# Performance work log

Hardware: AMD Instinct MI355X
Metric: run time of the kernel (lower is better)

The kernel has to match this reference:

```python
import jax, jax.numpy as jnp
import numpy as np

B, N, FEAT = 4, 100000, 11
NUM_SP = 512  # superpoints per sample
H1, H2, H3, E = 128, 256, 512, 384


def setup_inputs() -> dict:
    key = jax.random.key(0)
    ks = jax.random.split(key, 10)
    s = 0.02
    return {
        "full_features": jax.random.normal(ks[0], (B, N, FEAT), dtype=jnp.float32),
        "full_super_indices": jax.random.randint(ks[1], (B, N), 0, NUM_SP, dtype=jnp.int32),
        "W1": jax.random.normal(ks[2], (H1, FEAT), dtype=jnp.float32) * s,
        "b1": jnp.zeros((H1,), jnp.float32),
        "W2": jax.random.normal(ks[3], (H2, H1), dtype=jnp.float32) * s,
        "b2": jnp.zeros((H2,), jnp.float32),
        "W3": jax.random.normal(ks[4], (H3, H3), dtype=jnp.float32) * s,
        "b3": jnp.zeros((H3,), jnp.float32),
        "W4": jax.random.normal(ks[5], (E, H3), dtype=jnp.float32) * s,
        "b4": jnp.zeros((E,), jnp.float32),
    }


def reference(full_features, full_super_indices, W1, b1, W2, b2, W3, b3, W4, b4):
    # Vectorized form of the per-superpoint mini-PointNet:
    # conv1x1 MLP on points, segment-max pool, concat global+local, MLP, segment-max.
    x = full_features.reshape(B * N, FEAT)
    # first_conv: Conv1d(feat,128,1) -> Conv1d(128,256,1), no activation in between
    h = x @ W1.T + b1
    h = h @ W2.T + b2                                   # [B*N, 256]
    # global segment ids (batch-offset superpoint ids)
    seg = (full_super_indices.astype(jnp.int32) + jnp.arange(B, dtype=jnp.int32)[:, None] * NUM_SP).reshape(-1)
    gmax = jax.ops.segment_max(h, seg, num_segments=B * NUM_SP)  # [B*S, 256]
    g = gmax[seg]                                       # broadcast global feature back to points
    feat = jnp.concatenate([g, h], axis=-1)             # [B*N, 512] (global first, as in torch.cat)
    # second_conv: Conv1d(512,512,1) -> ReLU -> Conv1d(512,E,1)
    y = jax.nn.relu(feat @ W3.T + b3)
    y = y @ W4.T + b4                                   # [B*N, E]
    out = jax.ops.segment_max(y, seg, num_segments=B * NUM_SP)
    return out.reshape(B, NUM_SP, E)
```

## Files before the change

kernel.cpp:

```cpp
#include <hip/hip_runtime.h>
#include <hip/hip_bf16.h>
#include <math.h>

#define BB    4
#define NN    100000
#define NFEAT 11
#define NSP   512
#define NSEG  (BB*NSP)
#define NPTS  (BB*NN)
#define H2    256
#define H3    512
#define EE    384
#define MT    64
#define GS    (MT*8)
#define MI_N  (MT/16)
#define MAXL  15
#define RSEG  512
#define MAXS  12
#define ENCNI 0x007FFFFFu

typedef __attribute__((ext_vector_type(8))) short short8;
typedef __attribute__((ext_vector_type(4))) float f32x4;

__device__ __forceinline__ ushort f2bf(float f) {
  unsigned u = __builtin_bit_cast(unsigned, f);
  unsigned r = (u + 0x7FFFu + ((u >> 16) & 1u)) >> 16;
  return (ushort)r;
}
__device__ __forceinline__ unsigned encf(float f) {
  unsigned u = __builtin_bit_cast(unsigned, f);
  return u ^ ((unsigned)((int)u >> 31) | 0x80000000u);
}
__device__ __forceinline__ float decf(unsigned e) {
  unsigned u = (e & 0x80000000u) ? (e ^ 0x80000000u) : ~e;
  return __builtin_bit_cast(float, u);
}

__global__ void init_all(int* __restrict__ counts, int* __restrict__ cursor,
                         unsigned* __restrict__ gmaxEnc, unsigned* __restrict__ out_enc) {
  int i = blockIdx.x * 256 + threadIdx.x;
  if (i < NSEG * EE) out_enc[i] = ENCNI;
  if (i < NSEG * H2) gmaxEnc[i] = ENCNI;
  if (i < NSEG) { counts[i] = 0; cursor[i] = 0; }
}

__global__ void hist_kernel(const int* __restrict__ sidx, int* __restrict__ counts) {
  int i = blockIdx.x * blockDim.x + threadIdx.x;
  if (i < NPTS) {
    int seg = sidx[i] + (i / NN) * NSP;
    atomicAdd(&counts[seg], 1);
  }
}

__global__ void scan_kernel(const int* __restrict__ counts, int* __restrict__ offs) {
  __shared__ int buf[1024];
  int t = threadIdx.x;
  int c0 = counts[2 * t], c1 = counts[2 * t + 1];
  int s = c0 + c1;
  buf[t] = s;
  __syncthreads();
  for (int d = 1; d < 1024; d <<= 1) {
    int add = (t >= d) ? buf[t - d] : 0;
    __syncthreads();
    buf[t] += add;
    __syncthreads();
  }
  int incl = buf[t];
  int excl = incl - s;
  offs[2 * t] = excl;
  offs[2 * t + 1] = excl + c0;
  if (t == 1023) offs[2048] = incl;
}

__global__ void scatter_kernel(const int* __restrict__ sidx, const int* __restrict__ offs,
                               int* __restrict__ cursor, int* __restrict__ perm,
                               int* __restrict__ segp) {
  int i = blockIdx.x * blockDim.x + threadIdx.x;
  if (i < NPTS) {
    int seg = sidx[i] + (i / NN) * NSP;
    int pos = offs[seg] + atomicAdd(&cursor[seg], 1);
    perm[pos] = i;
    segp[pos] = seg;
  }
}

__global__ void prep_weights(const float* __restrict__ W1, const float* __restrict__ b1,
                             const float* __restrict__ W2, const float* __restrict__ b2,
                             const float* __restrict__ W3, const float* __restrict__ W4,
                             float* __restrict__ W12, float* __restrict__ b12,
                             float* __restrict__ W3gT, ushort* __restrict__ W3hP,
                             ushort* __restrict__ W4P) {
  int u = blockIdx.x * blockDim.x + threadIdx.x;
  if (u < H2 * NFEAT) {
    int c = u / NFEAT, f = u - c * NFEAT;
    float acc = 0.f;
    for (int j = 0; j < 128; ++j) acc += W2[c * 128 + j] * W1[j * NFEAT + f];
    W12[u] = acc;
  } else if (u < 3072) {
    int c = u - H2 * NFEAT;
    float acc = b2[c];
    for (int j = 0; j < 128; ++j) acc += W2[c * 128 + j] * b1[j];
    b12[c] = acc;
  } else if (u < 3072 + 131072) {
    int v = u - 3072;
    int c = v >> 9, o = v & 511;
    W3gT[v] = W3[o * H3 + c];
  } else if (u < 134144 + 16384) {
    int v = u - 134144;
    int ks = v >> 11, rem = v & 2047;
    int nt = rem >> 6, l = rem & 63;
    int n = nt * 16 + (l & 15);
    #pragma unroll
    for (int j = 0; j < 8; ++j) {
      int k = ks * 32 + (l >> 4) * 8 + j;
      W3hP[(size_t)v * 8 + j] = f2bf(W3[n * H3 + H2 + k]);
    }
  } else if (u < 150528 + 24576) {
    int v = u - 150528;
    int ks = v / 1536, rem = v - ks * 1536;
    int nt = rem >> 6, l = rem & 63;
    int n = nt * 16 + (l & 15);
    #pragma unroll
    for (int j = 0; j < 8; ++j) {
      int k = ks * 32 + (l >> 4) * 8 + j;
      W4P[(size_t)v * 8 + j] = f2bf(W4[n * H3 + k]);
    }
  }
}

__global__ __launch_bounds__(512) void gmax_kernel(
    const float* __restrict__ x, const int* __restrict__ perm,
    const int* __restrict__ segp,
    const float* __restrict__ W12, const float* __restrict__ b12,
    unsigned* __restrict__ gmaxEnc) {
  __shared__ float xs[RSEG * NFEAT];
  __shared__ float W12s[H2 * NFEAT];
  __shared__ float b12s[H2];
  __shared__ int   segd[RSEG];
  __shared__ unsigned gmaxL[MAXS * H2];

  const int t = threadIdx.x;
  const int mbeg = blockIdx.x * RSEG;
  const int nvalid = min(RSEG, NPTS - mbeg);

  for (int u = t; u < RSEG * NFEAT; u += 512) {
    int p = u / NFEAT, f = u - p * NFEAT;
    xs[u] = (p < nvalid) ? x[(size_t)perm[mbeg + p] * NFEAT + f] : 0.f;
  }
  for (int u = t; u < H2 * NFEAT; u += 512) W12s[u] = W12[u];
  if (t < H2) b12s[t] = b12[t];
  segd[t] = (t < nvalid) ? segp[mbeg + t] : segp[mbeg + nvalid - 1];
  for (int u = t; u < MAXS * H2; u += 512) gmaxL[u] = ENCNI;
  __syncthreads();

  const int s_lo = segd[0];
  const int s_hi = segd[nvalid - 1];
  const bool fb = (s_hi - s_lo + 1) > MAXS;

  const int g  = t >> 4;
  const int r0 = t & 15;
  const int cb = g * 8;

  float w12r[8][NFEAT], bbr[8];
  #pragma unroll
  for (int cj = 0; cj < 8; ++cj) {
    bbr[cj] = b12s[cb + cj];
    #pragma unroll
    for (int f = 0; f < NFEAT; ++f) w12r[cj][f] = W12s[(cb + cj) * NFEAT + f];
  }

  float m[8];
  #pragma unroll
  for (int cj = 0; cj < 8; ++cj) m[cj] = -INFINITY;
  int cur = segd[r0];
  bool any = false;

  for (int k = 0; k < 32; ++k) {
    int row = r0 + k * 16;
    if (row >= nvalid) break;
    int sg = segd[row];
    if (sg != cur) {
      #pragma unroll
      for (int cj = 0; cj < 8; ++cj) {
        unsigned e = encf(m[cj]);
        if (fb) atomicMax(&gmaxEnc[(size_t)cur * H2 + cb + cj], e);
        else    atomicMax(&gmaxL[(cur - s_lo) * H2 + cb + cj], e);
      }
      cur = sg;
      #pragma unroll
      for (int cj = 0; cj < 8; ++cj) m[cj] = -INFINITY;
    }
    float acc[8];
    #pragma unroll
    for (int cj = 0; cj < 8; ++cj) acc[cj] = bbr[cj];
    #pragma unroll
    for (int f = 0; f < NFEAT; ++f) {
      float xv = xs[row * NFEAT + f];
      #pragma unroll
      for (int cj = 0; cj < 8; ++cj) acc[cj] += w12r[cj][f] * xv;
    }
    #pragma unroll
    for (int cj = 0; cj < 8; ++cj) m[cj] = fmaxf(m[cj], acc[cj]);
    any = true;
  }
  if (any) {
    #pragma unroll
    for (int cj = 0; cj < 8; ++cj) {
      unsigned e = encf(m[cj]);
      if (fb) atomicMax(&gmaxEnc[(size_t)cur * H2 + cb + cj], e);
      else    atomicMax(&gmaxL[(cur - s_lo) * H2 + cb + cj], e);
    }
  }

  __syncthreads();
  if (!fb) {
    int nloc = s_hi - s_lo + 1;
    for (int u = t; u < nloc * H2; u += 512) {
      int sg = s_lo + (u >> 8);
      unsigned v = gmaxL[u];
      if (sg > s_lo && sg < s_hi) gmaxEnc[(size_t)sg * H2 + (u & 255)] = v;
      else atomicMax(&gmaxEnc[(size_t)sg * H2 + (u & 255)], v);
    }
  }
}

__global__ __launch_bounds__(256) void gpart_kernel(
    const unsigned* __restrict__ gmaxEnc, const float* __restrict__ W3gT,
    const float* __restrict__ b3, float* __restrict__ gpartG) {
  __shared__ float gm[8 * 256];
  const int t = threadIdx.x;
  const int b = blockIdx.x;
  for (int u = t; u < 8 * 256; u += 256) gm[u] = decf(gmaxEnc[(size_t)b * 8 * 256 + u]);
  __syncthreads();
  const float bb0 = b3[t], bb1 = b3[t + 256];
  float a0[8], a1[8];
  #pragma unroll
  for (int sg = 0; sg < 8; ++sg) { a0[sg] = bb0; a1[sg] = bb1; }
  for (int c = 0; c < 256; ++c) {
    float w0 = W3gT[c * 512 + t], w1 = W3gT[c * 512 + t + 256];
    #pragma unroll
    for (int sg = 0; sg < 8; ++sg) {
      float gv = gm[sg * 256 + c];
      a0[sg] += w0 * gv; a1[sg] += w1 * gv;
    }
  }
  #pragma unroll
  for (int sg = 0; sg < 8; ++sg) {
    size_t s = (size_t)b * 8 + sg;
    gpartG[s * 512 + t] = a0[sg];
    gpartG[s * 512 + t + 256] = a1[sg];
  }
}

__global__ void finalize_kernel(const unsigned* __restrict__ enc, float* __restrict__ out) {
  int i = blockIdx.x * 256 + threadIdx.x;
  if (i < NSEG * EE) out[i] = decf(enc[i]);
}

__global__ __launch_bounds__(512, 4) void main_kernel(
    const float* __restrict__ x, const int* __restrict__ perm,
    const int* __restrict__ segp,
    const float* __restrict__ W12, const float* __restrict__ b12,
    const ushort* __restrict__ W3hP, const ushort* __restrict__ W4P,
    const float* __restrict__ gpartG, const float* __restrict__ b4,
    unsigned* __restrict__ out_enc) {
  __shared__ __align__(16) ushort hsE[MT * 256];
  __shared__ __align__(16) ushort regB[MT * 256];
  __shared__ float gpartL[MAXL * 256];
  __shared__ int segdL[MT];
  __shared__ int s_loS, nlocS;

  const int t = threadIdx.x;
  const int w = t >> 6;
  const int l = t & 63;
  const int mbeg = blockIdx.x * MT;
  const int nvalid = min(MT, NPTS - mbeg);

  float* xsF  = (float*)regB;
  float* W12s = xsF + 704;
  float* b12s = W12s + 2816;
  ushort* y1E = regB;
  unsigned* obuf = (unsigned*)regB;

  for (int u = t; u < MT * NFEAT; u += 512) {
    int p = u / NFEAT, f = u - p * NFEAT;
    xsF[u] = (p < nvalid) ? x[(size_t)perm[mbeg + p] * NFEAT + f] : 0.f;
  }
  for (int u = t; u < 2816; u += 512) W12s[u] = W12[u];
  if (t < 256) b12s[t] = b12[t];
  if (t < MT) segdL[t] = (t < nvalid) ? segp[mbeg + t] : 0;
  __syncthreads();
  if (t == 0) {
    s_loS = segdL[0];
    nlocS = segdL[nvalid - 1] - segdL[0] + 1;
  }
  __syncthreads();
  const int s_lo = s_loS;
  const int nloc = nlocS;
  const bool fb = (nloc > MAXL);
  if (t < MT && t >= nvalid) segdL[t] = s_lo;

  #pragma unroll
  for (int i = 0; i < 4; ++i) {
    int gran = i * 8 + w;
    int cb = gran * 8;
    int row = l;
    uint4 pkt = {0, 0, 0, 0};
    if (row < nvalid) {
      float acc[8];
      #pragma unroll
      for (int cj = 0; cj < 8; ++cj) acc[cj] = b12s[cb + cj];
      #pragma unroll
      for (int f = 0; f < NFEAT; ++f) {
        float xv = xsF[row * NFEAT + f];
        #pragma unroll
        for (int cj = 0; cj < 8; ++cj) acc[cj] += W12s[(cb + cj) * NFEAT + f] * xv;
      }
      pkt.x = (unsigned)f2bf(acc[0]) | ((unsigned)f2bf(acc[1]) << 16);
      pkt.y = (unsigned)f2bf(acc[2]) | ((unsigned)f2bf(acc[3]) << 16);
      pkt.z = (unsigned)f2bf(acc[4]) | ((unsigned)f2bf(acc[5]) << 16);
      pkt.w = (unsigned)f2bf(acc[6]) | ((unsigned)f2bf(acc[7]) << 16);
    }
    *(uint4*)&hsE[gran * GS + row * 8] = pkt;
  }
  __syncthreads();

  float b4v[3];
  #pragma unroll
  for (int ni = 0; ni < 3; ++ni) b4v[ni] = b4[w * 48 + ni * 16 + (l & 15)];

  f32x4 acc4[MI_N][3];
  #pragma unroll
  for (int mi = 0; mi < MI_N; ++mi)
    #pragma unroll
    for (int ni = 0; ni < 3; ++ni)
      acc4[mi][ni] = (f32x4){0.f, 0.f, 0.f, 0.f};

  #pragma unroll
  for (int hf = 0; hf < 2; ++hf) {
    if (!fb) {
      for (int u = t; u < nloc * 256; u += 512) {
        int sg = u >> 8, c = u & 255;
        gpartL[u] = gpartG[(size_t)(s_lo + sg) * 512 + hf * 256 + c];
      }
    }

    f32x4 acc3[MI_N][2];
    #pragma unroll
    for (int mi = 0; mi < MI_N; ++mi)
      #pragma unroll
      for (int ni = 0; ni < 2; ++ni)
        acc3[mi][ni] = (f32x4){0.f, 0.f, 0.f, 0.f};

    {
      short8 bcur[2][2], bnxt[2][2];
      #pragma unroll
      for (int c2 = 0; c2 < 2; ++c2)
        #pragma unroll
        for (int ni = 0; ni < 2; ++ni)
          bcur[c2][ni] = *(const short8*)&W3hP[(size_t)(((c2) * 32 + hf * 16 + w * 2 + ni) * 64 + l) * 8];
      #pragma unroll
      for (int kc = 0; kc < 4; ++kc) {
        if (kc < 3) {
          #pragma unroll
          for (int c2 = 0; c2 < 2; ++c2)
            #pragma unroll
            for (int ni = 0; ni < 2; ++ni)
              bnxt[c2][ni] = *(const short8*)&W3hP[(size_t)(((kc * 2 + 2 + c2) * 32 + hf * 16 + w * 2 + ni) * 64 + l) * 8];
        }
        #pragma unroll
        for (int c2 = 0; c2 < 2; ++c2) {
          const int ks = kc * 2 + c2;
          #pragma unroll
          for (int mi = 0; mi < MI_N; ++mi) {
            short8 a = *(const short8*)&hsE[(ks * 4 + (l >> 4)) * GS + (mi * 16 + (l & 15)) * 8];
            acc3[mi][0] = __builtin_amdgcn_mfma_f32_16x16x32_bf16(a, bcur[c2][0], acc3[mi][0], 0, 0, 0);
            acc3[mi][1] = __builtin_amdgcn_mfma_f32_16x16x32_bf16(a, bcur[c2][1], acc3[mi][1], 0, 0, 0);
          }
        }
        if (kc < 3) {
          #pragma unroll
          for (int c2 = 0; c2 < 2; ++c2)
            #pragma unroll
            for (int ni = 0; ni < 2; ++ni)
              bcur[c2][ni] = bnxt[c2][ni];
        }
      }
    }
    __syncthreads();

    #pragma unroll
    for (int mi = 0; mi < MI_N; ++mi)
      #pragma unroll
      for (int ni = 0; ni < 2; ++ni) {
        int colh = w * 32 + ni * 16 + (l & 15);
        #pragma unroll
        for (int r = 0; r < 4; ++r) {
          int row = mi * 16 + (l >> 4) * 4 + r;
          int sg = segdL[row];
          float bias = fb ? gpartG[(size_t)sg * 512 + hf * 256 + colh]
                          : gpartL[(sg - s_lo) * 256 + colh];
          float v = fmaxf(acc3[mi][ni][r] + bias, 0.f);
          y1E[(colh >> 3) * GS + row * 8 + (colh & 7)] = f2bf(v);
        }
      }
    __syncthreads();

    {
      short8 bcur[2][3], bnxt[2][3];
      #pragma unroll
      for (int c2 = 0; c2 < 2; ++c2)
        #pragma unroll
        for (int ni = 0; ni < 3; ++ni)
          bcur[c2][ni] = *(const short8*)&W4P[(size_t)(((hf * 8 + c2) * 24 + w * 3 + ni) * 64 + l) * 8];
      #pragma unroll
      for (int kc = 0; kc < 4; ++kc) {
        if (kc < 3) {
          #pragma unroll
          for (int c2 = 0; c2 < 2; ++c2)
            #pragma unroll
            for (int ni = 0; ni < 3; ++ni)
              bnxt[c2][ni] = *(const short8*)&W4P[(size_t)(((hf * 8 + kc * 2 + 2 + c2) * 24 + w * 3 + ni) * 64 + l) * 8];
        }
        #pragma unroll
        for (int c2 = 0; c2 < 2; ++c2) {
          const int ks = kc * 2 + c2;
          #pragma unroll
          for (int mi = 0; mi < MI_N; ++mi) {
            short8 a = *(const short8*)&y1E[(ks * 4 + (l >> 4)) * GS + (mi * 16 + (l & 15)) * 8];
            acc4[mi][0] = __builtin_amdgcn_mfma_f32_16x16x32_bf16(a, bcur[c2][0], acc4[mi][0], 0, 0, 0);
            acc4[mi][1] = __builtin_amdgcn_mfma_f32_16x16x32_bf16(a, bcur[c2][1], acc4[mi][1], 0, 0, 0);
            acc4[mi][2] = __builtin_amdgcn_mfma_f32_16x16x32_bf16(a, bcur[c2][2], acc4[mi][2], 0, 0, 0);
          }
        }
        if (kc < 3) {
          #pragma unroll
          for (int c2 = 0; c2 < 2; ++c2)
            #pragma unroll
            for (int ni = 0; ni < 3; ++ni)
              bcur[c2][ni] = bnxt[c2][ni];
        }
      }
    }
    __syncthreads();
  }

  if (!fb) {
    for (int u = t; u < nloc * EE; u += 512) obuf[u] = ENCNI;
    __syncthreads();
    #pragma unroll
    for (int mi = 0; mi < MI_N; ++mi)
      #pragma unroll
      for (int ni = 0; ni < 3; ++ni) {
        int col = w * 48 + ni * 16 + (l & 15);
        #pragma unroll
        for (int r = 0; r < 4; ++r) {
          int row = mi * 16 + (l >> 4) * 4 + r;
          if (row < nvalid) {
            unsigned e = encf(acc4[mi][ni][r] + b4v[ni]);
            atomicMax(&obuf[(segdL[row] - s_lo) * EE + col], e);
          }
        }
      }
    __syncthreads();
    for (int u = t; u < nloc * EE; u += 512) {
      unsigned e = obuf[u];
      if (e != ENCNI)
        atomicMax(&out_enc[(size_t)(s_lo + u / EE) * EE + (u % EE)], e);
    }
  } else {
    #pragma unroll
    for (int mi = 0; mi < MI_N; ++mi)
      #pragma unroll
      for (int ni = 0; ni < 3; ++ni) {
        int col = w * 48 + ni * 16 + (l & 15);
        #pragma unroll
        for (int r = 0; r < 4; ++r) {
          int row = mi * 16 + (l >> 4) * 4 + r;
          if (row < nvalid) {
            unsigned e = encf(acc4[mi][ni][r] + b4v[ni]);
            atomicMax(&out_enc[(size_t)segdL[row] * EE + col], e);
          }
        }
      }
  }
}

extern "C" void kernel_launch(void* const* d_in, const int* in_sizes, int n_in,
                              void* d_out, int out_size, void* d_ws, size_t ws_size,
                              hipStream_t stream) {
  (void)in_sizes; (void)n_in; (void)out_size; (void)ws_size;
  const float* x    = (const float*)d_in[0];
  const int*   sidx = (const int*)d_in[1];
  const float* W1   = (const float*)d_in[2];
  const float* b1   = (const float*)d_in[3];
  const float* W2   = (const float*)d_in[4];
  const float* b2   = (const float*)d_in[5];
  const float* W3   = (const float*)d_in[6];
  const float* b3   = (const float*)d_in[7];
  const float* W4   = (const float*)d_in[8];
  const float* b4   = (const float*)d_in[9];
  float* out = (float*)d_out;

  char* ws = (char*)d_ws;
  size_t off = 0;
  auto alloc = [&](size_t bytes) {
    void* p = ws + off;
    off = (off + bytes + 255) & ~(size_t)255;
    return p;
  };
  int*      counts  = (int*)alloc(NSEG * 4);
  int*      cursor  = (int*)alloc(NSEG * 4);
  int*      offs    = (int*)alloc((NSEG + 1) * 4);
  int*      perm    = (int*)alloc((size_t)NPTS * 4);
  int*      segp    = (int*)alloc((size_t)NPTS * 4);
  float*    W12     = (float*)alloc(H2 * NFEAT * 4);
  float*    b12     = (float*)alloc(H2 * 4);
  float*    W3gT    = (float*)alloc((size_t)H2 * H3 * 4);
  ushort*   W3hP    = (ushort*)alloc((size_t)131072 * 2);
  ushort*   W4P     = (ushort*)alloc((size_t)196608 * 2);
  unsigned* gmaxEnc = (unsigned*)alloc((size_t)NSEG * H2 * 4);
  float*    gpartG  = (float*)alloc((size_t)NSEG * H3 * 4);
  unsigned* out_enc = (unsigned*)alloc((size_t)NSEG * EE * 4);

  init_all<<<(NSEG * EE + 255) / 256, 256, 0, stream>>>(counts, cursor, gmaxEnc, out_enc);
  const int preptotal = 150528 + 24576;
  prep_weights<<<(preptotal + 255) / 256, 256, 0, stream>>>(W1, b1, W2, b2, W3, W4,
                                                            W12, b12, W3gT, W3hP, W4P);
  hist_kernel<<<(NPTS + 255) / 256, 256, 0, stream>>>(sidx, counts);
  scan_kernel<<<1, 1024, 0, stream>>>(counts, offs);
  scatter_kernel<<<(NPTS + 255) / 256, 256, 0, stream>>>(sidx, offs, cursor, perm, segp);
  gmax_kernel<<<(NPTS + RSEG - 1) / RSEG, 512, 0, stream>>>(x, perm, segp, W12, b12, gmaxEnc);
  gpart_kernel<<<NSEG / 8, 256, 0, stream>>>(gmaxEnc, W3gT, b3, gpartG);
  main_kernel<<<NPTS / MT, 512, 0, stream>>>(x, perm, segp, W12, b12,
                                             W3hP, W4P, gpartG, b4, out_enc);
  finalize_kernel<<<(NSEG * EE + 255) / 256, 256, 0, stream>>>(out_enc, out);
}
```

Baseline: 787.6 us.

## Materialize first-layer activations in bf16 from gmax pass and reuse in main kernel

The gmax kernel now writes the per-point 256-wide first-stage activations as bf16 into a workspace buffer, laid out in the MFMA-friendly tile order. A new main kernel loads them directly instead of regathering x through the permutation and recomputing the 11->256 projection. Its epilogue also pre-reduces the output max into a shared buffer when a tile spans few segments, which cuts global atomics. The cost is about 200MB of extra global write and read traffic, with a fallback to the old path when the workspace is too small.

After: 650.8 us. 17.4% less time.

```diff
diff --git a/kernel.cpp b/kernel.cpp
--- a/kernel.cpp
+++ b/kernel.cpp
@@ -128,11 +128,12 @@
   }
 }
 
+template <bool STOREH>
 __global__ __launch_bounds__(512) void gmax_kernel(
     const float* __restrict__ x, const int* __restrict__ perm,
     const int* __restrict__ segp,
     const float* __restrict__ W12, const float* __restrict__ b12,
-    unsigned* __restrict__ gmaxEnc) {
+    unsigned* __restrict__ gmaxEnc, ushort* __restrict__ hG) {
   __shared__ float xs[RSEG * NFEAT];
   __shared__ float W12s[H2 * NFEAT];
   __shared__ float b12s[H2];
@@ -198,6 +199,15 @@
       float xv = xs[row * NFEAT + f];
       #pragma unroll
       for (int cj = 0; cj < 8; ++cj) acc[cj] += w12r[cj][f] * xv;
+    }
+    if (STOREH) {
+      uint4 pkt;
+      pkt.x = (unsigned)f2bf(acc[0]) | ((unsigned)f2bf(acc[1]) << 16);
+      pkt.y = (unsigned)f2bf(acc[2]) | ((unsigned)f2bf(acc[3]) << 16);
+      pkt.z = (unsigned)f2bf(acc[4]) | ((unsigned)f2bf(acc[5]) << 16);
+      pkt.w = (unsigned)f2bf(acc[6]) | ((unsigned)f2bf(acc[7]) << 16);
+      int pt = mbeg + row;
+      *(uint4*)&hG[(size_t)(pt >> 6) * 16384 + ((size_t)g * 64 + (pt & 63)) * 8] = pkt;
     }
     #pragma unroll
     for (int cj = 0; cj < 8; ++cj) m[cj] = fmaxf(m[cj], acc[cj]);
@@ -255,6 +265,206 @@
 __global__ void finalize_kernel(const unsigned* __restrict__ enc, float* __restrict__ out) {
   int i = blockIdx.x * 256 + threadIdx.x;
   if (i < NSEG * EE) out[i] = decf(enc[i]);
+}
+
+__global__ __launch_bounds__(512, 4) void main_v2(
+    const int* __restrict__ segp, const ushort* __restrict__ hG,
+    const ushort* __restrict__ W3hP, const ushort* __restrict__ W4P,
+    const float* __restrict__ gpartG, const float* __restrict__ b4,
+    unsigned* __restrict__ out_enc) {
+  __shared__ __align__(16) ushort hsE[MT * 256];
+  __shared__ __align__(16) ushort regB[MT * 256];
+  __shared__ float gpartL[MAXL * 256];
+  __shared__ int segdL[MT];
+  __shared__ int s_loS, nlocS;
+
+  const int t = threadIdx.x;
+  const int w = t >> 6;
+  const int l = t & 63;
+  const int mbeg = blockIdx.x * MT;
+
+  ushort* y1E = regB;
+  unsigned* obuf = (unsigned*)regB;
+
+  {
+    const size_t tb = (size_t)blockIdx.x * (MT * 256);
+    #pragma unroll
+    for (int i = 0; i < 4; ++i)
+      *(uint4*)&hsE[(size_t)(i * 512 + t) * 8] = *(const uint4*)&hG[tb + (size_t)(i * 512 + t) * 8];
+  }
+  if (t < MT) segdL[t] = segp[mbeg + t];
+  __syncthreads();
+  if (t == 0) {
+    s_loS = segdL[0];
+    nlocS = segdL[MT - 1] - segdL[0] + 1;
+  }
+  __syncthreads();
+  const int s_lo = s_loS;
+  const int nloc = nlocS;
+  const bool fb = (nloc > MAXL);
+
+  float b4v[3];
+  #pragma unroll
+  for (int ni = 0; ni < 3; ++ni) b4v[ni] = b4[w * 48 + ni * 16 + (l & 15)];
+
+  f32x4 acc4[MI_N][3];
+  #pragma unroll
+  for (int mi = 0; mi < MI_N; ++mi)
+    #pragma unroll
+    for (int ni = 0; ni < 3; ++ni)
+      acc4[mi][ni] = (f32x4){0.f, 0.f, 0.f, 0.f};
+
+  #pragma unroll
+  for (int hf = 0; hf < 2; ++hf) {
+    if (!fb) {
+      for (int u = t; u < nloc * 256; u += 512) {
+        int sg = u >> 8, c = u & 255;
+        gpartL[u] = gpartG[(size_t)(s_lo + sg) * 512 + hf * 256 + c];
+      }
+    }
+
+    f32x4 acc3[MI_N][2];
+    #pragma unroll
+    for (int mi = 0; mi < MI_N; ++mi)
+      #pragma unroll
+      for (int ni = 0; ni < 2; ++ni)
+        acc3[mi][ni] = (f32x4){0.f, 0.f, 0.f, 0.f};
+
+    {
+      short8 bcur[2][2], bnxt[2][2];
+      #pragma unroll
+      for (int c2 = 0; c2 < 2; ++c2)
+        #pragma unroll
+        for (int ni = 0; ni < 2; ++ni)
+          bcur[c2][ni] = *(const short8*)&W3hP[(size_t)(((c2) * 32 + hf * 16 + w * 2 + ni) * 64 + l) * 8];
+      #pragma unroll
+      for (int kc = 0; kc < 4; ++kc) {
+        if (kc < 3) {
+          #pragma unroll
+          for (int c2 = 0; c2 < 2; ++c2)
+            #pragma unroll
+            for (int ni = 0; ni < 2; ++ni)
+              bnxt[c2][ni] = *(const short8*)&W3hP[(size_t)(((kc * 2 + 2 + c2) * 32 + hf * 16 + w * 2 + ni) * 64 + l) * 8];
+        }
+        #pragma unroll
+        for (int c2 = 0; c2 < 2; ++c2) {
+          const int ks = kc * 2 + c2;
+          #pragma unroll
+          for (int mi = 0; mi < MI_N; ++mi) {
+            short8 a = *(const short8*)&hsE[(ks * 4 + (l >> 4)) * GS + (mi * 16 + (l & 15)) * 8];
+            acc3[mi][0] = __builtin_amdgcn_mfma_f32_16x16x32_bf16(a, bcur[c2][0], acc3[mi][0], 0, 0, 0);
+            acc3[mi][1] = __builtin_amdgcn_mfma_f32_16x16x32_bf16(a, bcur[c2][1], acc3[mi][1], 0, 0, 0);
+          }
+        }
+        if (kc < 3) {
+          #pragma unroll
+          for (int c2 = 0; c2 < 2; ++c2)
+            #pragma unroll
+            for (int ni = 0; ni < 2; ++ni)
+              bcur[c2][ni] = bnxt[c2][ni];
+        }
+      }
+    }
+    __syncthreads();
+
+    #pragma unroll
+    for (int mi = 0; mi < MI_N; ++mi)
+      #pragma unroll
+      for (int ni = 0; ni < 2; ++ni) {
+        int colh = w * 32 + ni * 16 + (l & 15);
+        #pragma unroll
+        for (int r = 0; r < 4; ++r) {
+          int row = mi * 16 + (l >> 4) * 4 + r;
+          int sg = segdL[row];
+          float bias = fb ? gpartG[(size_t)sg * 512 + hf * 256 + colh]
+                          : gpartL[(sg - s_lo) * 256 + colh];
+          float v = fmaxf(acc3[mi][ni][r] + bias, 0.f);
+          y1E[(colh >> 3) * GS + row * 8 + (colh & 7)] = f2bf(v);
+        }
+      }
+    __syncthreads();
+
+    {
+      short8 bcur[2][3], bnxt[2][3];
+      #pragma unroll
+      for (int c2 = 0; c2 < 2; ++c2)
+        #pragma unroll
+        for (int ni = 0; ni < 3; ++ni)
+          bcur[c2][ni] = *(const short8*)&W4P[(size_t)(((hf * 8 + c2) * 24 + w * 3 + ni) * 64 + l) * 8];
+      #pragma unroll
+      for (int kc = 0; kc < 4; ++kc) {
+        if (kc < 3) {
+          #pragma unroll
+          for (int c2 = 0; c2 < 2; ++c2)
+            #pragma unroll
+            for (int ni = 0; ni < 3; ++ni)
+              bnxt[c2][ni] = *(const short8*)&W4P[(size_t)(((hf * 8 + kc * 2 + 2 + c2) * 24 + w * 3 + ni) * 64 + l) * 8];
+        }
+        #pragma unroll
+        for (int c2 = 0; c2 < 2; ++c2) {
+          const int ks = kc * 2 + c2;
+          #pragma unroll
+          for (int mi = 0; mi < MI_N; ++mi) {
+            short8 a = *(const short8*)&y1E[(ks * 4 + (l >> 4)) * GS + (mi * 16 + (l & 15)) * 8];
+            acc4[mi][0] = __builtin_amdgcn_mfma_f32_16x16x32_bf16(a, bcur[c2][0], acc4[mi][0], 0, 0, 0);
+            acc4[mi][1] = __builtin_amdgcn_mfma_f32_16x16x32_bf16(a, bcur[c2][1], acc4[mi][1], 0, 0, 0);
+            acc4[mi][2] = __builtin_amdgcn_mfma_f32_16x16x32_bf16(a, bcur[c2][2], acc4[mi][2], 0, 0, 0);
+          }
+        }
+        if (kc < 3) {
+          #pragma unroll
+          for (int c2 = 0; c2 < 2; ++c2)
+            #pragma unroll
+            for (int ni = 0; ni < 3; ++ni)
+              bcur[c2][ni] = bnxt[c2][ni];
+        }
+      }
+    }
+    __syncthreads();
+  }
+
+  if (!fb) {
+    for (int u = t; u < nloc * EE; u += 512) obuf[u] = ENCNI;
+    __syncthreads();
+    #pragma unroll
+    for (int mi = 0; mi < MI_N; ++mi) {
+      int rbase = mi * 16 + (l >> 4) * 4;
+      int sg0 = segdL[rbase], sg3 = segdL[rbase + 3];
+      #pragma unroll
+      for (int ni = 0; ni < 3; ++ni) {
+        int col = w * 48 + ni * 16 + (l & 15);
+        if (sg0 == sg3) {
+          float m4 = fmaxf(fmaxf(acc4[mi][ni][0], acc4[mi][ni][1]),
+                           fmaxf(acc4[mi][ni][2], acc4[mi][ni][3]));
+          atomicMax(&obuf[(sg0 - s_lo) * EE + col], encf(m4 + b4v[ni]));
+        } else {
+          #pragma unroll
+          for (int r = 0; r < 4; ++r)
+            atomicMax(&obuf[(segdL[rbase + r] - s_lo) * EE + col],
+                      encf(acc4[mi][ni][r] + b4v[ni]));
+        }
+      }
+    }
+    __syncthreads();
+    for (int u = t; u < nloc * EE; u += 512) {
+      unsigned e = obuf[u];
+      if (e != ENCNI)
+        atomicMax(&out_enc[(size_t)(s_lo + u / EE) * EE + (u % EE)], e);
+    }
+  } else {
+    #pragma unroll
+    for (int mi = 0; mi < MI_N; ++mi)
+      #pragma unroll
+      for (int ni = 0; ni < 3; ++ni) {
+        int col = w * 48 + ni * 16 + (l & 15);
+        #pragma unroll
+        for (int r = 0; r < 4; ++r) {
+          int row = mi * 16 + (l >> 4) * 4 + r;
+          unsigned e = encf(acc4[mi][ni][r] + b4v[ni]);
+          atomicMax(&out_enc[(size_t)segdL[row] * EE + col], e);
+        }
+      }
+  }
 }
 
 __global__ __launch_bounds__(512, 4) void main_kernel(
@@ -489,7 +699,7 @@
 extern "C" void kernel_launch(void* const* d_in, const int* in_sizes, int n_in,
                               void* d_out, int out_size, void* d_ws, size_t ws_size,
                               hipStream_t stream) {
-  (void)in_sizes; (void)n_in; (void)out_size; (void)ws_size;
+  (void)in_sizes; (void)n_in; (void)out_size;
   const float* x    = (const float*)d_in[0];
   const int*   sidx = (const int*)d_in[1];
   const float* W1   = (const float*)d_in[2];
@@ -522,6 +732,8 @@
   unsigned* gmaxEnc = (unsigned*)alloc((size_t)NSEG * H2 * 4);
   float*    gpartG  = (float*)alloc((size_t)NSEG * H3 * 4);
   unsigned* out_enc = (unsigned*)alloc((size_t)NSEG * EE * 4);
+  ushort*   hG      = (ushort*)alloc((size_t)NPTS * 256 * 2);
+  const bool useH = (off <= ws_size);
 
   init_all<<<(NSEG * EE + 255) / 256, 256, 0, stream>>>(counts, cursor, gmaxEnc, out_enc);
   const int preptotal = 150528 + 24576;
@@ -530,9 +742,15 @@
   hist_kernel<<<(NPTS + 255) / 256, 256, 0, stream>>>(sidx, counts);
   scan_kernel<<<1, 1024, 0, stream>>>(counts, offs);
   scatter_kernel<<<(NPTS + 255) / 256, 256, 0, stream>>>(sidx, offs, cursor, perm, segp);
-  gmax_kernel<<<(NPTS + RSEG - 1) / RSEG, 512, 0, stream>>>(x, perm, segp, W12, b12, gmaxEnc);
-  gpart_kernel<<<NSEG / 8, 256, 0, stream>>>(gmaxEnc, W3gT, b3, gpartG);
-  main_kernel<<<NPTS / MT, 512, 0, stream>>>(x, perm, segp, W12, b12,
-                                             W3hP, W4P, gpartG, b4, out_enc);
+  if (useH) {
+    gmax_kernel<true><<<(NPTS + RSEG - 1) / RSEG, 512, 0, stream>>>(x, perm, segp, W12, b12, gmaxEnc, hG);
+    gpart_kernel<<<NSEG / 8, 256, 0, stream>>>(gmaxEnc, W3gT, b3, gpartG);
+    main_v2<<<NPTS / MT, 512, 0, stream>>>(segp, hG, W3hP, W4P, gpartG, b4, out_enc);
+  } else {
+    gmax_kernel<false><<<(NPTS + RSEG - 1) / RSEG, 512, 0, stream>>>(x, perm, segp, W12, b12, gmaxEnc, hG);
+    gpart_kernel<<<NSEG / 8, 256, 0, stream>>>(gmaxEnc, W3gT, b3, gpartG);
+    main_kernel<<<NPTS / MT, 512, 0, stream>>>(x, perm, segp, W12, b12,
+                                               W3hP, W4P, gpartG, b4, out_enc);
+  }
   finalize_kernel<<<(NSEG * EE + 255) / 256, 256, 0, stream>>>(out_enc, out);
 }
```
